# Performance work log

Measured on AMD Instinct MI355X. Metric: run time of the kernel, lower is better.

Reference implementation:

```python
import jax, jax.numpy as jnp
import numpy as np

N = 500000      # examples = M * (nr+1)
K = 20          # context set size (indices[:, 3:])
NR = 24         # negatives per positive
H = 128         # hidden_channels == node feature dim
NODES = 10000   # ingredient vocabulary


def setup_inputs() -> dict:
    key = jax.random.key(0)
    ks = jax.random.split(key, 6)
    indices = jax.random.randint(ks[0], (N, 3 + K), 0, NODES)
    x = jax.random.normal(ks[1], (NODES, H), dtype=jnp.float32)
    scale = 0.02
    W1 = jax.random.normal(ks[2], (H, 3 * H), dtype=jnp.float32) * scale
    b1 = jnp.zeros((H,), jnp.float32)
    W2 = jax.random.normal(ks[3], (H // 2, H), dtype=jnp.float32) * scale
    b2 = jnp.zeros((H // 2,), jnp.float32)
    W3 = jax.random.normal(ks[4], (1, H // 2), dtype=jnp.float32) * scale
    b3 = jnp.zeros((1,), jnp.float32)
    return {"indices": indices, "nr": NR, "x": x,
            "W1": W1, "b1": b1, "W2": W2, "b2": b2, "W3": W3, "b3": b3}


def _embed_context(ctx_idx, x, nr):
    # ctx_idx: [N, K]; one context row per group of (nr+1) examples
    new_idx = ctx_idx[:-1:nr + 1]                 # [M, K]
    emb = x[new_idx]                               # [M, K, H] gather
    s = emb.sum(axis=1)                            # [M, H]
    norm = jnp.maximum((new_idx > 0).sum(axis=1), 1).astype(x.dtype)[:, None]
    mean = s / norm                                # masked mean over context
    return jnp.repeat(mean, nr + 1, axis=0)        # broadcast back to [N, H]


def reference(indices, nr, x, W1, b1, W2, b2, W3, b3):
    ing1 = x[indices[:, 0]]                        # [N, H]
    ing2 = x[indices[:, 1]]                        # [N, H]
    set_emb = _embed_context(indices[:, 3:], x, nr)  # [N, H]
    y = jnp.concatenate([ing1, ing2, set_emb], axis=1)  # [N, 3H]
    y = jax.nn.relu(y @ W1.T + b1)
    y = jax.nn.relu(y @ W2.T + b2)
    return y @ W3.T + b3                           # [N, 1]
```

## Files before the change

### kernel.cpp

```cpp
#include <hip/hip_runtime.h>
#include <hip/hip_bf16.h>

#define N_ROWS   500000
#define NR1      25
#define NGROUPS  20000
#define KCTX     20
#define H        128
#define NODES    10000
#define IDX_COLS 23

#define RPB      128
#define MAXG     7

typedef __attribute__((ext_vector_type(8))) short short8;
typedef __attribute__((ext_vector_type(4))) float f32x4;

__device__ __forceinline__ unsigned pkbf(float lo, float hi) {
  __hip_bfloat162 h = __float22bfloat162_rn(make_float2(lo, hi));
  union { __hip_bfloat162 h; unsigned u; } c; c.h = h;
  return c.u;
}
__device__ __forceinline__ float bf2f(unsigned short u) {
  union { unsigned u; float f; } c; c.u = ((unsigned)u) << 16; return c.f;
}

#define GPB 8
#define MEAN_BLOCKS (NGROUPS / GPB)
__global__ __launch_bounds__(256) void k_means(
    const int* __restrict__ indices, const float* __restrict__ x,
    unsigned short* __restrict__ gm) {
  const int tid = threadIdx.x;
  const int sub = tid >> 6;
  const int jj  = (tid & 63) * 2;
#pragma unroll
  for (int it = 0; it < GPB / 4; ++it) {
    const int g = blockIdx.x * GPB + it * 4 + sub;
    const int* __restrict__ rowidx =
        indices + (size_t)g * NR1 * IDX_COLS + 3;
    float s0 = 0.f, s1 = 0.f;
    int cnt = 0;
#pragma unroll
    for (int c = 0; c < KCTX; ++c) {
      const int idx = rowidx[c];
      const float2 v = *(const float2*)(x + (size_t)idx * H + jj);
      s0 += v.x; s1 += v.y;
      cnt += (idx > 0) ? 1 : 0;
    }
    const float rn = 1.f / (float)((cnt > 1) ? cnt : 1);
    *(unsigned*)(gm + (size_t)g * H + jj) = pkbf(s0 * rn, s1 * rn);
  }
}

#define PN 64
#define PBLK  ((NODES + PN - 1) / PN)
#define GBLK  ((NGROUPS + PN - 1) / PN)
#define B_PG  (4 * PBLK)
#define B_IDX (B_PG + 2 * GBLK)
#define PRE_BLOCKS (B_IDX + PBLK)

__global__ __launch_bounds__(256) void k_precompute(
    const float* __restrict__ x, const float* __restrict__ W1,
    const float* __restrict__ b1, const unsigned short* __restrict__ gm,
    const int* __restrict__ indices,
    unsigned short* __restrict__ Pb, float* __restrict__ Pg,
    int2* __restrict__ idx2) {
  const int tid = threadIdx.x;
  const int bid = blockIdx.x;

  if (bid >= B_IDX) {
    const int stride = PBLK * 256;
    for (int r = (bid - B_IDX) * 256 + tid; r < N_ROWS; r += stride) {
      idx2[r] = make_int2(indices[(size_t)r * IDX_COLS + 0],
                          indices[(size_t)r * IDX_COLS + 1]);
    }
    return;
  }

  __shared__ short wlds[64][136];

  const bool isPg = (bid >= B_PG);
  int m, sub;
  if (isPg) { m = 2; sub = bid - B_PG; }
  else      { m = bid / (2 * PBLK); sub = bid - m * (2 * PBLK); }
  const int tbase = (sub >> 1) * PN;
  const int ch    = sub & 1;

#pragma unroll
  for (int it = 0; it < 8; ++it) {
    const int f  = it * 256 + tid;
    const int j  = f >> 5;
    const int q4 = f & 31;
    const float4 v =
        *(const float4*)(W1 + (size_t)(ch * 64 + j) * (3 * H) + m * H + q4 * 4);
    *(unsigned*)&wlds[j][q4 * 4]     = pkbf(v.x, v.y);
    *(unsigned*)&wlds[j][q4 * 4 + 2] = pkbf(v.z, v.w);
  }
  __syncthreads();

  const int lane = tid & 63;
  const int wv   = tid >> 6;
  const int col  = lane & 15;
  const int quad = lane >> 4;

  short8 Af[4];
  if (isPg) {
    int g = tbase + wv * 16 + col;
    if (g > NGROUPS - 1) g = NGROUPS - 1;
    const short8* __restrict__ gr = (const short8*)(gm + (size_t)g * H);
#pragma unroll
    for (int kt = 0; kt < 4; ++kt) Af[kt] = gr[kt * 4 + quad];
  } else {
    int node = tbase + wv * 16 + col;
    if (node > NODES - 1) node = NODES - 1;
    const float4* __restrict__ xr = (const float4*)(x + (size_t)node * H);
#pragma unroll
    for (int kt = 0; kt < 4; ++kt) {
      const int f4 = kt * 8 + quad * 2;
      const float4 v0 = xr[f4], v1 = xr[f4 + 1];
      union { short8 v; unsigned u[4]; } pk;
      pk.u[0] = pkbf(v0.x, v0.y);
      pk.u[1] = pkbf(v0.z, v0.w);
      pk.u[2] = pkbf(v1.x, v1.y);
      pk.u[3] = pkbf(v1.z, v1.w);
      Af[kt] = pk.v;
    }
  }

  f32x4 acc[4];
#pragma unroll
  for (int ct = 0; ct < 4; ++ct) acc[ct] = (f32x4)(0.f);

#pragma unroll
  for (int kt = 0; kt < 4; ++kt) {
#pragma unroll
    for (int ct = 0; ct < 4; ++ct) {
      const short8 Bf = *(const short8*)&wlds[ct * 16 + col][kt * 32 + quad * 8];
      acc[ct] = __builtin_amdgcn_mfma_f32_16x16x32_bf16(Af[kt], Bf, acc[ct], 0, 0, 0);
    }
  }

  if (isPg) {
    float b1v[4];
#pragma unroll
    for (int ct = 0; ct < 4; ++ct) b1v[ct] = b1[ch * 64 + ct * 16 + col];
#pragma unroll
    for (int reg = 0; reg < 4; ++reg) {
      const int g = tbase + wv * 16 + quad * 4 + reg;
      if (g < NGROUPS) {
#pragma unroll
        for (int ct = 0; ct < 4; ++ct)
          Pg[(size_t)g * H + ch * 64 + ct * 16 + col] = acc[ct][reg] + b1v[ct];
      }
    }
  } else {
    unsigned short* __restrict__ Pm = Pb + (size_t)m * NODES * H;
#pragma unroll
    for (int reg = 0; reg < 4; ++reg) {
      const int n = tbase + wv * 16 + quad * 4 + reg;
      if (n < NODES) {
#pragma unroll
        for (int ct = 0; ct < 4; ++ct) {
          union { unsigned u; unsigned short s[2]; } c;
          c.u = pkbf(acc[ct][reg], 0.f);
          Pm[(size_t)n * H + ch * 64 + ct * 16 + col] = c.s[0];
        }
      }
    }
  }
}

__global__ __launch_bounds__(256) void k_main(
    const int2* __restrict__ idx2,
    const unsigned short* __restrict__ P1b, const unsigned short* __restrict__ P2b,
    const float* __restrict__ Pg,
    const float* __restrict__ W2, const float* __restrict__ b2,
    const float* __restrict__ W3, const float* __restrict__ b3,
    float* __restrict__ out) {
  __shared__ short w2s[64][136];
  __shared__ float cgs[MAXG][132];

  const int tid   = threadIdx.x;
  const int rbase = blockIdx.x * RPB;
  const int gbase = rbase / NR1;

  const int lane = tid & 63;
  const int wv   = tid >> 6;
  const int col  = lane & 15;
  const int quad = lane >> 4;

  short8 ua[2][4], ub[2][4];
  int    gl[2];
  {
    const int R = rbase + wv * 32;
#pragma unroll
    for (int rt = 0; rt < 2; ++rt) {
      const int r  = R + rt * 16 + col;
      const int rc = (r < N_ROWS) ? r : (N_ROWS - 1);
      const int2 ii = idx2[rc];
      const short8* __restrict__ pa = (const short8*)(P1b + (size_t)ii.x * H);
      const short8* __restrict__ pb = (const short8*)(P2b + (size_t)ii.y * H);
#pragma unroll
      for (int kt = 0; kt < 4; ++kt) {
        ua[rt][kt] = pa[kt * 4 + quad];
        ub[rt][kt] = pb[kt * 4 + quad];
      }
      gl[rt] = rc / NR1 - gbase;
    }
  }

  for (int idx = tid; idx < 64 * 64; idx += 256) {
    const int n  = idx >> 6;
    const int kp = idx & 63;
    const float2 w = *(const float2*)(W2 + (size_t)n * H + kp * 2);
    *(unsigned*)&w2s[n][kp * 2] = pkbf(w.x, w.y);
  }

  {
    int rlast = rbase + RPB - 1; if (rlast > N_ROWS - 1) rlast = N_ROWS - 1;
    const int G = rlast / NR1 - gbase + 1;
    const float* __restrict__ Pgrow = Pg + (size_t)gbase * H;
    for (int i = tid; i < G * 32; i += 256) {
      const int g = i >> 5;
      const int c = (i & 31) * 4;
      *(float4*)&cgs[g][c] = *(const float4*)(Pgrow + (size_t)g * H + c);
    }
  }
  __syncthreads();

  float b2v[4], w3v[4];
#pragma unroll
  for (int ct = 0; ct < 4; ++ct) {
    b2v[ct] = b2[ct * 16 + col];
    w3v[ct] = W3[ct * 16 + col];
  }
  const float bias3 = b3[0];

  short8 A[2][4];
#pragma unroll
  for (int rt = 0; rt < 2; ++rt) {
#pragma unroll
    for (int kt = 0; kt < 4; ++kt) {
      union { short8 v; unsigned short s[8]; } va, vb;
      va.v = ua[rt][kt];
      vb.v = ub[rt][kt];
      const float4 c0 = *(const float4*)&cgs[gl[rt]][kt * 32 + quad * 8];
      const float4 c1 = *(const float4*)&cgs[gl[rt]][kt * 32 + quad * 8 + 4];
      const float h0 = fmaxf(bf2f(va.s[0]) + bf2f(vb.s[0]) + c0.x, 0.f);
      const float h1 = fmaxf(bf2f(va.s[1]) + bf2f(vb.s[1]) + c0.y, 0.f);
      const float h2 = fmaxf(bf2f(va.s[2]) + bf2f(vb.s[2]) + c0.z, 0.f);
      const float h3 = fmaxf(bf2f(va.s[3]) + bf2f(vb.s[3]) + c0.w, 0.f);
      const float h4 = fmaxf(bf2f(va.s[4]) + bf2f(vb.s[4]) + c1.x, 0.f);
      const float h5 = fmaxf(bf2f(va.s[5]) + bf2f(vb.s[5]) + c1.y, 0.f);
      const float h6 = fmaxf(bf2f(va.s[6]) + bf2f(vb.s[6]) + c1.z, 0.f);
      const float h7 = fmaxf(bf2f(va.s[7]) + bf2f(vb.s[7]) + c1.w, 0.f);
      union { short8 v; unsigned u[4]; } pk;
      pk.u[0] = pkbf(h0, h1);
      pk.u[1] = pkbf(h2, h3);
      pk.u[2] = pkbf(h4, h5);
      pk.u[3] = pkbf(h6, h7);
      A[rt][kt] = pk.v;
    }
  }

  f32x4 acc[2][4];
#pragma unroll
  for (int rt = 0; rt < 2; ++rt)
#pragma unroll
    for (int ct = 0; ct < 4; ++ct) acc[rt][ct] = (f32x4)(0.f);
#pragma unroll
  for (int kt = 0; kt < 4; ++kt) {
#pragma unroll
    for (int ct = 0; ct < 4; ++ct) {
      const short8 Bf = *(const short8*)&w2s[ct * 16 + col][kt * 32 + quad * 8];
#pragma unroll
      for (int rt = 0; rt < 2; ++rt)
        acc[rt][ct] = __builtin_amdgcn_mfma_f32_16x16x32_bf16(
            A[rt][kt], Bf, acc[rt][ct], 0, 0, 0);
    }
  }

  const int Rt = rbase + wv * 32;
#pragma unroll
  for (int rt = 0; rt < 2; ++rt) {
#pragma unroll
    for (int reg = 0; reg < 4; ++reg) {
      float s = 0.f;
#pragma unroll
      for (int ct = 0; ct < 4; ++ct)
        s += fmaxf(acc[rt][ct][reg] + b2v[ct], 0.f) * w3v[ct];
      s += __shfl_xor(s, 1);
      s += __shfl_xor(s, 2);
      s += __shfl_xor(s, 4);
      s += __shfl_xor(s, 8);
      if (col == 0) {
        const int row = Rt + rt * 16 + quad * 4 + reg;
        if (row < N_ROWS) out[row] = s + bias3;
      }
    }
  }
}

extern "C" void kernel_launch(void* const* d_in, const int* in_sizes, int n_in,
                              void* d_out, int out_size, void* d_ws, size_t ws_size,
                              hipStream_t stream) {
  const int*   indices = (const int*)  d_in[0];
  const float* x  = (const float*)d_in[2];
  const float* W1 = (const float*)d_in[3];
  const float* b1 = (const float*)d_in[4];
  const float* W2 = (const float*)d_in[5];
  const float* b2 = (const float*)d_in[6];
  const float* W3 = (const float*)d_in[7];
  const float* b3 = (const float*)d_in[8];
  float* out = (float*)d_out;

  unsigned short* Pb  = (unsigned short*)d_ws;
  unsigned short* P1b = Pb;
  unsigned short* P2b = Pb + (size_t)NODES * H;
  unsigned short* gm  = Pb + (size_t)2 * NODES * H;
  float* Pg   = (float*)(gm + (size_t)NGROUPS * H);
  int2*  idx2 = (int2*)(Pg + (size_t)NGROUPS * H);

  k_means<<<MEAN_BLOCKS, 256, 0, stream>>>(indices, x, gm);
  k_precompute<<<PRE_BLOCKS, 256, 0, stream>>>(x, W1, b1, gm, indices,
                                               Pb, Pg, idx2);
  k_main<<<(N_ROWS + RPB - 1) / RPB, 256, 0, stream>>>(idx2, P1b, P2b, Pg,
                                                       W2, b2, W3, b3, out);
}
```

Before: 177.7 us.

## Process two row tiles per block with prefetch and XOR-swizzled LDS weights

k_main now covers 256 rows per block as two 128-row tiles. The second tile's P1/P2 gathers are issued before the first tile's compute, so gather latency overlaps the MFMA work. The padded LDS weight arrays are replaced with an XOR-swizzled 128-wide layout to avoid bank conflicts, and W2 is loaded with float4. In exchange this halves the block count and raises register pressure, which may lower occupancy.

```diff
diff --git a/kernel.cpp b/kernel.cpp
--- a/kernel.cpp
+++ b/kernel.cpp
@@ -9,8 +9,9 @@
 #define NODES    10000
 #define IDX_COLS 23
 
-#define RPB      128
-#define MAXG     7
+#define RPB      256
+#define NT       2
+#define MAXG     12
 
 typedef __attribute__((ext_vector_type(8))) short short8;
 typedef __attribute__((ext_vector_type(4))) float f32x4;
@@ -76,7 +77,7 @@
     return;
   }
 
-  __shared__ short wlds[64][136];
+  __shared__ __align__(16) short wlds[64 * 128];
 
   const bool isPg = (bid >= B_PG);
   int m, sub;
@@ -92,8 +93,9 @@
     const int q4 = f & 31;
     const float4 v =
         *(const float4*)(W1 + (size_t)(ch * 64 + j) * (3 * H) + m * H + q4 * 4);
-    *(unsigned*)&wlds[j][q4 * 4]     = pkbf(v.x, v.y);
-    *(unsigned*)&wlds[j][q4 * 4 + 2] = pkbf(v.z, v.w);
+    const int sidx = j * 128 + (((q4 >> 1) ^ (j & 7)) << 3) + (q4 & 1) * 4;
+    *(unsigned*)&wlds[sidx]     = pkbf(v.x, v.y);
+    *(unsigned*)&wlds[sidx + 2] = pkbf(v.z, v.w);
   }
   __syncthreads();
 
@@ -134,7 +136,9 @@
   for (int kt = 0; kt < 4; ++kt) {
 #pragma unroll
     for (int ct = 0; ct < 4; ++ct) {
-      const short8 Bf = *(const short8*)&wlds[ct * 16 + col][kt * 32 + quad * 8];
+      const int brow = ct * 16 + col;
+      const short8 Bf = *(const short8*)
+          &wlds[brow * 128 + (((kt * 4 + quad) ^ (brow & 7)) << 3)];
       acc[ct] = __builtin_amdgcn_mfma_f32_16x16x32_bf16(Af[kt], Bf, acc[ct], 0, 0, 0);
     }
   }
@@ -176,8 +180,8 @@
     const float* __restrict__ W2, const float* __restrict__ b2,
     const float* __restrict__ W3, const float* __restrict__ b3,
     float* __restrict__ out) {
-  __shared__ short w2s[64][136];
-  __shared__ float cgs[MAXG][132];
+  __shared__ __align__(16) short w2s[64 * 128];
+  __shared__ float cgs[MAXG][128];
 
   const int tid   = threadIdx.x;
   const int rbase = blockIdx.x * RPB;
@@ -188,31 +192,42 @@
   const int col  = lane & 15;
   const int quad = lane >> 4;
 
-  short8 ua[2][4], ub[2][4];
-  int    gl[2];
+  short8 ua[2][2][4], ub[2][2][4];
+  int    gl[2][2];
+  int2   ii1[2];
   {
-    const int R = rbase + wv * 32;
+    const int R0 = rbase + wv * 32;
+    const int R1 = R0 + 128;
+    int rc0[2], rc1[2];
 #pragma unroll
     for (int rt = 0; rt < 2; ++rt) {
-      const int r  = R + rt * 16 + col;
-      const int rc = (r < N_ROWS) ? r : (N_ROWS - 1);
-      const int2 ii = idx2[rc];
-      const short8* __restrict__ pa = (const short8*)(P1b + (size_t)ii.x * H);
-      const short8* __restrict__ pb = (const short8*)(P2b + (size_t)ii.y * H);
+      int r0 = R0 + rt * 16 + col; rc0[rt] = (r0 < N_ROWS) ? r0 : (N_ROWS - 1);
+      int r1 = R1 + rt * 16 + col; rc1[rt] = (r1 < N_ROWS) ? r1 : (N_ROWS - 1);
+    }
+    int2 ii0[2];
+#pragma unroll
+    for (int rt = 0; rt < 2; ++rt) { ii0[rt] = idx2[rc0[rt]]; ii1[rt] = idx2[rc1[rt]]; }
+#pragma unroll
+    for (int rt = 0; rt < 2; ++rt) {
+      const short8* __restrict__ pa = (const short8*)(P1b + (size_t)ii0[rt].x * H);
+      const short8* __restrict__ pb = (const short8*)(P2b + (size_t)ii0[rt].y * H);
 #pragma unroll
       for (int kt = 0; kt < 4; ++kt) {
-        ua[rt][kt] = pa[kt * 4 + quad];
-        ub[rt][kt] = pb[kt * 4 + quad];
-      }
-      gl[rt] = rc / NR1 - gbase;
-    }
-  }
-
-  for (int idx = tid; idx < 64 * 64; idx += 256) {
-    const int n  = idx >> 6;
-    const int kp = idx & 63;
-    const float2 w = *(const float2*)(W2 + (size_t)n * H + kp * 2);
-    *(unsigned*)&w2s[n][kp * 2] = pkbf(w.x, w.y);
+        ua[0][rt][kt] = pa[kt * 4 + quad];
+        ub[0][rt][kt] = pb[kt * 4 + quad];
+      }
+      gl[0][rt] = rc0[rt] / NR1 - gbase;
+      gl[1][rt] = rc1[rt] / NR1 - gbase;
+    }
+  }
+
+  for (int i = tid; i < 2048; i += 256) {
+    const int n  = i >> 5;
+    const int q4 = i & 31;
+    const float4 w = *(const float4*)(W2 + (size_t)n * H + q4 * 4);
+    const int sidx = n * 128 + (((q4 >> 1) ^ (n & 7)) << 3) + (q4 & 1) * 4;
+    *(unsigned*)&w2s[sidx]     = pkbf(w.x, w.y);
+    *(unsigned*)&w2s[sidx + 2] = pkbf(w.z, w.w);
   }
 
   {
@@ -235,66 +250,87 @@
   }
   const float bias3 = b3[0];
 
-  short8 A[2][4];
-#pragma unroll
-  for (int rt = 0; rt < 2; ++rt) {
+#pragma unroll
+  for (int t = 0; t < NT; ++t) {
+    const int cur = t & 1;
+
+    if (t + 1 < NT) {
+      const int nxt = cur ^ 1;
+#pragma unroll
+      for (int rt = 0; rt < 2; ++rt) {
+        const short8* __restrict__ pa = (const short8*)(P1b + (size_t)ii1[rt].x * H);
+        const short8* __restrict__ pb = (const short8*)(P2b + (size_t)ii1[rt].y * H);
+#pragma unroll
+        for (int kt = 0; kt < 4; ++kt) {
+          ua[nxt][rt][kt] = pa[kt * 4 + quad];
+          ub[nxt][rt][kt] = pb[kt * 4 + quad];
+        }
+      }
+    }
+
+    short8 A[2][4];
+#pragma unroll
+    for (int rt = 0; rt < 2; ++rt) {
+#pragma unroll
+      for (int kt = 0; kt < 4; ++kt) {
+        union { short8 v; unsigned short s[8]; } va, vb;
+        va.v = ua[cur][rt][kt];
+        vb.v = ub[cur][rt][kt];
+        const float4 c0 = *(const float4*)&cgs[gl[cur][rt]][kt * 32 + quad * 8];
+        const float4 c1 = *(const float4*)&cgs[gl[cur][rt]][kt * 32 + quad * 8 + 4];
+        const float h0 = fmaxf(bf2f(va.s[0]) + bf2f(vb.s[0]) + c0.x, 0.f);
+        const float h1 = fmaxf(bf2f(va.s[1]) + bf2f(vb.s[1]) + c0.y, 0.f);
+        const float h2 = fmaxf(bf2f(va.s[2]) + bf2f(vb.s[2]) + c0.z, 0.f);
+        const float h3 = fmaxf(bf2f(va.s[3]) + bf2f(vb.s[3]) + c0.w, 0.f);
+        const float h4 = fmaxf(bf2f(va.s[4]) + bf2f(vb.s[4]) + c1.x, 0.f);
+        const float h5 = fmaxf(bf2f(va.s[5]) + bf2f(vb.s[5]) + c1.y, 0.f);
+        const float h6 = fmaxf(bf2f(va.s[6]) + bf2f(vb.s[6]) + c1.z, 0.f);
+        const float h7 = fmaxf(bf2f(va.s[7]) + bf2f(vb.s[7]) + c1.w, 0.f);
+        union { short8 v; unsigned u[4]; } pk;
+        pk.u[0] = pkbf(h0, h1);
+        pk.u[1] = pkbf(h2, h3);
+        pk.u[2] = pkbf(h4, h5);
+        pk.u[3] = pkbf(h6, h7);
+        A[rt][kt] = pk.v;
+      }
+    }
+
+    f32x4 acc[2][4];
+#pragma unroll
+    for (int rt = 0; rt < 2; ++rt)
+#pragma unroll
+      for (int ct = 0; ct < 4; ++ct) acc[rt][ct] = (f32x4)(0.f);
 #pragma unroll
     for (int kt = 0; kt < 4; ++kt) {
-      union { short8 v; unsigned short s[8]; } va, vb;
-      va.v = ua[rt][kt];
-      vb.v = ub[rt][kt];
-      const float4 c0 = *(const float4*)&cgs[gl[rt]][kt * 32 + quad * 8];
-      const float4 c1 = *(const float4*)&cgs[gl[rt]][kt * 32 + quad * 8 + 4];
-      const float h0 = fmaxf(bf2f(va.s[0]) + bf2f(vb.s[0]) + c0.x, 0.f);
-      const float h1 = fmaxf(bf2f(va.s[1]) + bf2f(vb.s[1]) + c0.y, 0.f);
-      const float h2 = fmaxf(bf2f(va.s[2]) + bf2f(vb.s[2]) + c0.z, 0.f);
-      const float h3 = fmaxf(bf2f(va.s[3]) + bf2f(vb.s[3]) + c0.w, 0.f);
-      const float h4 = fmaxf(bf2f(va.s[4]) + bf2f(vb.s[4]) + c1.x, 0.f);
-      const float h5 = fmaxf(bf2f(va.s[5]) + bf2f(vb.s[5]) + c1.y, 0.f);
-      const float h6 = fmaxf(bf2f(va.s[6]) + bf2f(vb.s[6]) + c1.z, 0.f);
-      const float h7 = fmaxf(bf2f(va.s[7]) + bf2f(vb.s[7]) + c1.w, 0.f);
-      union { short8 v; unsigned u[4]; } pk;
-      pk.u[0] = pkbf(h0, h1);
-      pk.u[1] = pkbf(h2, h3);
-      pk.u[2] = pkbf(h4, h5);
-      pk.u[3] = pkbf(h6, h7);
-      A[rt][kt] = pk.v;
-    }
-  }
-
-  f32x4 acc[2][4];
-#pragma unroll
-  for (int rt = 0; rt < 2; ++rt)
-#pragma unroll
-    for (int ct = 0; ct < 4; ++ct) acc[rt][ct] = (f32x4)(0.f);
-#pragma unroll
-  for (int kt = 0; kt < 4; ++kt) {
-#pragma unroll
-    for (int ct = 0; ct < 4; ++ct) {
-      const short8 Bf = *(const short8*)&w2s[ct * 16 + col][kt * 32 + quad * 8];
-#pragma unroll
-      for (int rt = 0; rt < 2; ++rt)
-        acc[rt][ct] = __builtin_amdgcn_mfma_f32_16x16x32_bf16(
-            A[rt][kt], Bf, acc[rt][ct], 0, 0, 0);
-    }
-  }
-
-  const int Rt = rbase + wv * 32;
-#pragma unroll
-  for (int rt = 0; rt < 2; ++rt) {
-#pragma unroll
-    for (int reg = 0; reg < 4; ++reg) {
-      float s = 0.f;
-#pragma unroll
-      for (int ct = 0; ct < 4; ++ct)
-        s += fmaxf(acc[rt][ct][reg] + b2v[ct], 0.f) * w3v[ct];
-      s += __shfl_xor(s, 1);
-      s += __shfl_xor(s, 2);
-      s += __shfl_xor(s, 4);
-      s += __shfl_xor(s, 8);
-      if (col == 0) {
-        const int row = Rt + rt * 16 + quad * 4 + reg;
-        if (row < N_ROWS) out[row] = s + bias3;
+#pragma unroll
+      for (int ct = 0; ct < 4; ++ct) {
+        const int brow = ct * 16 + col;
+        const short8 Bf = *(const short8*)
+            &w2s[brow * 128 + (((kt * 4 + quad) ^ (brow & 7)) << 3)];
+#pragma unroll
+        for (int rt = 0; rt < 2; ++rt)
+          acc[rt][ct] = __builtin_amdgcn_mfma_f32_16x16x32_bf16(
+              A[rt][kt], Bf, acc[rt][ct], 0, 0, 0);
+      }
+    }
+
+    const int Rt = rbase + t * 128 + wv * 32;
+#pragma unroll
+    for (int rt = 0; rt < 2; ++rt) {
+#pragma unroll
+      for (int reg = 0; reg < 4; ++reg) {
+        float s = 0.f;
+#pragma unroll
+        for (int ct = 0; ct < 4; ++ct)
+          s += fmaxf(acc[rt][ct][reg] + b2v[ct], 0.f) * w3v[ct];
+        s += __shfl_xor(s, 1);
+        s += __shfl_xor(s, 2);
+        s += __shfl_xor(s, 4);
+        s += __shfl_xor(s, 8);
+        if (col == 0) {
+          const int row = Rt + rt * 16 + quad * 4 + reg;
+          if (row < N_ROWS) out[row] = s + bias3;
+        }
       }
     }
   }
```

New measurement: 168.5 us. -5.1%, faster.

## Drop LDS staging in main kernel, prepack W2 fragments, read indices directly

Applied to the files above, without the earlier changes.

The main kernel no longer stages W2 and the per-group context projections in shared memory or synchronises. W2 is pre-converted once into MFMA-ready bf16 fragments that each lane loads straight from global memory, and the context rows are read directly per row. The separate idx2 compaction pass is removed, so the main kernel reads columns 0 and 1 of indices with a strided access. Each wave now handles 16 rows instead of 32, with 4 blocks per CU requested. The W1 shared-memory tile in precompute switches to an XOR-swizzled layout to avoid bank conflicts. The trade is more redundant global and L2 traffic per row in exchange for no barrier or LDS fill and higher occupancy.

```diff
diff --git a/kernel.cpp b/kernel.cpp
--- a/kernel.cpp
+++ b/kernel.cpp
@@ -9,9 +9,6 @@
 #define NODES    10000
 #define IDX_COLS 23
 
-#define RPB      128
-#define MAXG     7
-
 typedef __attribute__((ext_vector_type(8))) short short8;
 typedef __attribute__((ext_vector_type(4))) float f32x4;
 
@@ -20,8 +17,11 @@
   union { __hip_bfloat162 h; unsigned u; } c; c.h = h;
   return c.u;
 }
-__device__ __forceinline__ float bf2f(unsigned short u) {
-  union { unsigned u; float f; } c; c.u = ((unsigned)u) << 16; return c.f;
+__device__ __forceinline__ float lo2f(unsigned u) {
+  union { unsigned u; float f; } c; c.u = u << 16; return c.f;
+}
+__device__ __forceinline__ float hi2f(unsigned u) {
+  union { unsigned u; float f; } c; c.u = u & 0xffff0000u; return c.f;
 }
 
 #define GPB 8
@@ -55,28 +55,43 @@
 #define PBLK  ((NODES + PN - 1) / PN)
 #define GBLK  ((NGROUPS + PN - 1) / PN)
 #define B_PG  (4 * PBLK)
-#define B_IDX (B_PG + 2 * GBLK)
-#define PRE_BLOCKS (B_IDX + PBLK)
+#define B_W2F (B_PG + 2 * GBLK)
+#define PRE_BLOCKS (B_W2F + 1)
 
 __global__ __launch_bounds__(256) void k_precompute(
     const float* __restrict__ x, const float* __restrict__ W1,
     const float* __restrict__ b1, const unsigned short* __restrict__ gm,
-    const int* __restrict__ indices,
+    const float* __restrict__ W2,
     unsigned short* __restrict__ Pb, float* __restrict__ Pg,
-    int2* __restrict__ idx2) {
+    unsigned short* __restrict__ w2f) {
   const int tid = threadIdx.x;
   const int bid = blockIdx.x;
 
-  if (bid >= B_IDX) {
-    const int stride = PBLK * 256;
-    for (int r = (bid - B_IDX) * 256 + tid; r < N_ROWS; r += stride) {
-      idx2[r] = make_int2(indices[(size_t)r * IDX_COLS + 0],
-                          indices[(size_t)r * IDX_COLS + 1]);
+  const int lane = tid & 63;
+  const int wvid = tid >> 6;
+  const int col  = lane & 15;
+  const int quad = lane >> 4;
+
+  if (bid == B_W2F) {
+#pragma unroll
+    for (int i = 0; i < 4; ++i) {
+      const int fi = i * 4 + wvid;
+      const int kt = fi >> 2, ct = fi & 3;
+      const float* __restrict__ src =
+          W2 + (size_t)(ct * 16 + col) * H + kt * 32 + quad * 8;
+      const float4 v0 = *(const float4*)src;
+      const float4 v1 = *(const float4*)(src + 4);
+      union { short8 v; unsigned u[4]; } pk;
+      pk.u[0] = pkbf(v0.x, v0.y);
+      pk.u[1] = pkbf(v0.z, v0.w);
+      pk.u[2] = pkbf(v1.x, v1.y);
+      pk.u[3] = pkbf(v1.z, v1.w);
+      *(short8*)(w2f + (size_t)(fi * 64 + lane) * 8) = pk.v;
     }
     return;
   }
 
-  __shared__ short wlds[64][136];
+  __shared__ __align__(16) short wlds[64 * 128];
 
   const bool isPg = (bid >= B_PG);
   int m, sub;
@@ -92,25 +107,21 @@
     const int q4 = f & 31;
     const float4 v =
         *(const float4*)(W1 + (size_t)(ch * 64 + j) * (3 * H) + m * H + q4 * 4);
-    *(unsigned*)&wlds[j][q4 * 4]     = pkbf(v.x, v.y);
-    *(unsigned*)&wlds[j][q4 * 4 + 2] = pkbf(v.z, v.w);
+    const int sidx = j * 128 + (((q4 >> 1) ^ (j & 7)) << 3) + (q4 & 1) * 4;
+    *(unsigned*)&wlds[sidx]     = pkbf(v.x, v.y);
+    *(unsigned*)&wlds[sidx + 2] = pkbf(v.z, v.w);
   }
   __syncthreads();
-
-  const int lane = tid & 63;
-  const int wv   = tid >> 6;
-  const int col  = lane & 15;
-  const int quad = lane >> 4;
 
   short8 Af[4];
   if (isPg) {
-    int g = tbase + wv * 16 + col;
+    int g = tbase + wvid * 16 + col;
     if (g > NGROUPS - 1) g = NGROUPS - 1;
     const short8* __restrict__ gr = (const short8*)(gm + (size_t)g * H);
 #pragma unroll
     for (int kt = 0; kt < 4; ++kt) Af[kt] = gr[kt * 4 + quad];
   } else {
-    int node = tbase + wv * 16 + col;
+    int node = tbase + wvid * 16 + col;
     if (node > NODES - 1) node = NODES - 1;
     const float4* __restrict__ xr = (const float4*)(x + (size_t)node * H);
 #pragma unroll
@@ -134,7 +145,9 @@
   for (int kt = 0; kt < 4; ++kt) {
 #pragma unroll
     for (int ct = 0; ct < 4; ++ct) {
-      const short8 Bf = *(const short8*)&wlds[ct * 16 + col][kt * 32 + quad * 8];
+      const int brow = ct * 16 + col;
+      const short8 Bf = *(const short8*)
+          &wlds[brow * 128 + (((kt * 4 + quad) ^ (brow & 7)) << 3)];
       acc[ct] = __builtin_amdgcn_mfma_f32_16x16x32_bf16(Af[kt], Bf, acc[ct], 0, 0, 0);
     }
   }
@@ -145,7 +158,7 @@
     for (int ct = 0; ct < 4; ++ct) b1v[ct] = b1[ch * 64 + ct * 16 + col];
 #pragma unroll
     for (int reg = 0; reg < 4; ++reg) {
-      const int g = tbase + wv * 16 + quad * 4 + reg;
+      const int g = tbase + wvid * 16 + quad * 4 + reg;
       if (g < NGROUPS) {
 #pragma unroll
         for (int ct = 0; ct < 4; ++ct)
@@ -156,7 +169,7 @@
     unsigned short* __restrict__ Pm = Pb + (size_t)m * NODES * H;
 #pragma unroll
     for (int reg = 0; reg < 4; ++reg) {
-      const int n = tbase + wv * 16 + quad * 4 + reg;
+      const int n = tbase + wvid * 16 + quad * 4 + reg;
       if (n < NODES) {
 #pragma unroll
         for (int ct = 0; ct < 4; ++ct) {
@@ -169,63 +182,42 @@
   }
 }
 
-__global__ __launch_bounds__(256) void k_main(
-    const int2* __restrict__ idx2,
+__global__ __launch_bounds__(256, 4) void k_main(
+    const int* __restrict__ indices,
     const unsigned short* __restrict__ P1b, const unsigned short* __restrict__ P2b,
-    const float* __restrict__ Pg,
-    const float* __restrict__ W2, const float* __restrict__ b2,
-    const float* __restrict__ W3, const float* __restrict__ b3,
-    float* __restrict__ out) {
-  __shared__ short w2s[64][136];
-  __shared__ float cgs[MAXG][132];
-
-  const int tid   = threadIdx.x;
-  const int rbase = blockIdx.x * RPB;
-  const int gbase = rbase / NR1;
-
+    const float* __restrict__ Pg, const unsigned short* __restrict__ w2f,
+    const float* __restrict__ b2, const float* __restrict__ W3,
+    const float* __restrict__ b3, float* __restrict__ out) {
+  const int tid  = threadIdx.x;
   const int lane = tid & 63;
   const int wv   = tid >> 6;
   const int col  = lane & 15;
   const int quad = lane >> 4;
 
-  short8 ua[2][4], ub[2][4];
-  int    gl[2];
-  {
-    const int R = rbase + wv * 32;
-#pragma unroll
-    for (int rt = 0; rt < 2; ++rt) {
-      const int r  = R + rt * 16 + col;
-      const int rc = (r < N_ROWS) ? r : (N_ROWS - 1);
-      const int2 ii = idx2[rc];
-      const short8* __restrict__ pa = (const short8*)(P1b + (size_t)ii.x * H);
-      const short8* __restrict__ pb = (const short8*)(P2b + (size_t)ii.y * H);
-#pragma unroll
-      for (int kt = 0; kt < 4; ++kt) {
-        ua[rt][kt] = pa[kt * 4 + quad];
-        ub[rt][kt] = pb[kt * 4 + quad];
-      }
-      gl[rt] = rc / NR1 - gbase;
-    }
-  }
-
-  for (int idx = tid; idx < 64 * 64; idx += 256) {
-    const int n  = idx >> 6;
-    const int kp = idx & 63;
-    const float2 w = *(const float2*)(W2 + (size_t)n * H + kp * 2);
-    *(unsigned*)&w2s[n][kp * 2] = pkbf(w.x, w.y);
-  }
-
-  {
-    int rlast = rbase + RPB - 1; if (rlast > N_ROWS - 1) rlast = N_ROWS - 1;
-    const int G = rlast / NR1 - gbase + 1;
-    const float* __restrict__ Pgrow = Pg + (size_t)gbase * H;
-    for (int i = tid; i < G * 32; i += 256) {
-      const int g = i >> 5;
-      const int c = (i & 31) * 4;
-      *(float4*)&cgs[g][c] = *(const float4*)(Pgrow + (size_t)g * H + c);
-    }
-  }
-  __syncthreads();
+  const int Rw = (blockIdx.x * 4 + wv) * 16;
+  const int r  = Rw + col;
+  const int rc = (r < N_ROWS) ? r : (N_ROWS - 1);
+
+  const int i0 = indices[(size_t)rc * IDX_COLS + 0];
+  const int i1 = indices[(size_t)rc * IDX_COLS + 1];
+  const int g  = rc / NR1;
+
+  const short8* __restrict__ pa = (const short8*)(P1b + (size_t)i0 * H);
+  const short8* __restrict__ pb = (const short8*)(P2b + (size_t)i1 * H);
+  short8 ua[4], ub[4];
+#pragma unroll
+  for (int kt = 0; kt < 4; ++kt) {
+    ua[kt] = pa[kt * 4 + quad];
+    ub[kt] = pb[kt * 4 + quad];
+  }
+
+  const float* __restrict__ cg = Pg + (size_t)g * H;
+  float4 c0[4], c1[4];
+#pragma unroll
+  for (int kt = 0; kt < 4; ++kt) {
+    c0[kt] = *(const float4*)(cg + kt * 32 + quad * 8);
+    c1[kt] = *(const float4*)(cg + kt * 32 + quad * 8 + 4);
+  }
 
   float b2v[4], w3v[4];
 #pragma unroll
@@ -235,67 +227,53 @@
   }
   const float bias3 = b3[0];
 
-  short8 A[2][4];
-#pragma unroll
-  for (int rt = 0; rt < 2; ++rt) {
-#pragma unroll
-    for (int kt = 0; kt < 4; ++kt) {
-      union { short8 v; unsigned short s[8]; } va, vb;
-      va.v = ua[rt][kt];
-      vb.v = ub[rt][kt];
-      const float4 c0 = *(const float4*)&cgs[gl[rt]][kt * 32 + quad * 8];
-      const float4 c1 = *(const float4*)&cgs[gl[rt]][kt * 32 + quad * 8 + 4];
-      const float h0 = fmaxf(bf2f(va.s[0]) + bf2f(vb.s[0]) + c0.x, 0.f);
-      const float h1 = fmaxf(bf2f(va.s[1]) + bf2f(vb.s[1]) + c0.y, 0.f);
-      const float h2 = fmaxf(bf2f(va.s[2]) + bf2f(vb.s[2]) + c0.z, 0.f);
-      const float h3 = fmaxf(bf2f(va.s[3]) + bf2f(vb.s[3]) + c0.w, 0.f);
-      const float h4 = fmaxf(bf2f(va.s[4]) + bf2f(vb.s[4]) + c1.x, 0.f);
-      const float h5 = fmaxf(bf2f(va.s[5]) + bf2f(vb.s[5]) + c1.y, 0.f);
-      const float h6 = fmaxf(bf2f(va.s[6]) + bf2f(vb.s[6]) + c1.z, 0.f);
-      const float h7 = fmaxf(bf2f(va.s[7]) + bf2f(vb.s[7]) + c1.w, 0.f);
-      union { short8 v; unsigned u[4]; } pk;
-      pk.u[0] = pkbf(h0, h1);
-      pk.u[1] = pkbf(h2, h3);
-      pk.u[2] = pkbf(h4, h5);
-      pk.u[3] = pkbf(h6, h7);
-      A[rt][kt] = pk.v;
-    }
-  }
-
-  f32x4 acc[2][4];
-#pragma unroll
-  for (int rt = 0; rt < 2; ++rt)
-#pragma unroll
-    for (int ct = 0; ct < 4; ++ct) acc[rt][ct] = (f32x4)(0.f);
+  short8 A[4];
+#pragma unroll
+  for (int kt = 0; kt < 4; ++kt) {
+    union { short8 v; unsigned u[4]; } va, vb;
+    va.v = ua[kt]; vb.v = ub[kt];
+    const float h0 = fmaxf(lo2f(va.u[0]) + lo2f(vb.u[0]) + c0[kt].x, 0.f);
+    const float h1 = fmaxf(hi2f(va.u[0]) + hi2f(vb.u[0]) + c0[kt].y, 0.f);
+    const float h2 = fmaxf(lo2f(va.u[1]) + lo2f(vb.u[1]) + c0[kt].z, 0.f);
+    const float h3 = fmaxf(hi2f(va.u[1]) + hi2f(vb.u[1]) + c0[kt].w, 0.f);
+    const float h4 = fmaxf(lo2f(va.u[2]) + lo2f(vb.u[2]) + c1[kt].x, 0.f);
+    const float h5 = fmaxf(hi2f(va.u[2]) + hi2f(vb.u[2]) + c1[kt].y, 0.f);
+    const float h6 = fmaxf(lo2f(va.u[3]) + lo2f(vb.u[3]) + c1[kt].z, 0.f);
+    const float h7 = fmaxf(hi2f(va.u[3]) + hi2f(vb.u[3]) + c1[kt].w, 0.f);
+    union { short8 v; unsigned u[4]; } pk;
+    pk.u[0] = pkbf(h0, h1);
+    pk.u[1] = pkbf(h2, h3);
+    pk.u[2] = pkbf(h4, h5);
+    pk.u[3] = pkbf(h6, h7);
+    A[kt] = pk.v;
+  }
+
+  f32x4 acc[4];
+#pragma unroll
+  for (int ct = 0; ct < 4; ++ct) acc[ct] = (f32x4)(0.f);
 #pragma unroll
   for (int kt = 0; kt < 4; ++kt) {
 #pragma unroll
     for (int ct = 0; ct < 4; ++ct) {
-      const short8 Bf = *(const short8*)&w2s[ct * 16 + col][kt * 32 + quad * 8];
-#pragma unroll
-      for (int rt = 0; rt < 2; ++rt)
-        acc[rt][ct] = __builtin_amdgcn_mfma_f32_16x16x32_bf16(
-            A[rt][kt], Bf, acc[rt][ct], 0, 0, 0);
-    }
-  }
-
-  const int Rt = rbase + wv * 32;
-#pragma unroll
-  for (int rt = 0; rt < 2; ++rt) {
-#pragma unroll
-    for (int reg = 0; reg < 4; ++reg) {
-      float s = 0.f;
-#pragma unroll
-      for (int ct = 0; ct < 4; ++ct)
-        s += fmaxf(acc[rt][ct][reg] + b2v[ct], 0.f) * w3v[ct];
-      s += __shfl_xor(s, 1);
-      s += __shfl_xor(s, 2);
-      s += __shfl_xor(s, 4);
-      s += __shfl_xor(s, 8);
-      if (col == 0) {
-        const int row = Rt + rt * 16 + quad * 4 + reg;
-        if (row < N_ROWS) out[row] = s + bias3;
-      }
+      const short8 Bf =
+          *(const short8*)(w2f + (size_t)((kt * 4 + ct) * 64 + lane) * 8);
+      acc[ct] = __builtin_amdgcn_mfma_f32_16x16x32_bf16(A[kt], Bf, acc[ct], 0, 0, 0);
+    }
+  }
+
+#pragma unroll
+  for (int reg = 0; reg < 4; ++reg) {
+    float s = 0.f;
+#pragma unroll
+    for (int ct = 0; ct < 4; ++ct)
+      s += fmaxf(acc[ct][reg] + b2v[ct], 0.f) * w3v[ct];
+    s += __shfl_xor(s, 1);
+    s += __shfl_xor(s, 2);
+    s += __shfl_xor(s, 4);
+    s += __shfl_xor(s, 8);
+    if (col == 0) {
+      const int row = Rw + quad * 4 + reg;
+      if (row < N_ROWS) out[row] = s + bias3;
     }
   }
 }
@@ -317,12 +295,11 @@
   unsigned short* P1b = Pb;
   unsigned short* P2b = Pb + (size_t)NODES * H;
   unsigned short* gm  = Pb + (size_t)2 * NODES * H;
-  float* Pg   = (float*)(gm + (size_t)NGROUPS * H);
-  int2*  idx2 = (int2*)(Pg + (size_t)NGROUPS * H);
+  float* Pg = (float*)(gm + (size_t)NGROUPS * H);
+  unsigned short* w2f = (unsigned short*)(Pg + (size_t)NGROUPS * H);
 
   k_means<<<MEAN_BLOCKS, 256, 0, stream>>>(indices, x, gm);
-  k_precompute<<<PRE_BLOCKS, 256, 0, stream>>>(x, W1, b1, gm, indices,
-                                               Pb, Pg, idx2);
-  k_main<<<(N_ROWS + RPB - 1) / RPB, 256, 0, stream>>>(idx2, P1b, P2b, Pg,
-                                                       W2, b2, W3, b3, out);
-}
+  k_precompute<<<PRE_BLOCKS, 256, 0, stream>>>(x, W1, b1, gm, W2, Pb, Pg, w2f);
+  k_main<<<(N_ROWS + 63) / 64, 256, 0, stream>>>(indices, P1b, P2b, Pg, w2f,
+                                                 b2, W3, b3, out);
+}
```

Result: faster. 169.9 us (-4.4%).
